# Optimization experiments

Hardware: AMD Instinct MI355X
Metric: run time of the kernel (lower is better)

Reference implementation:

```python
import jax, jax.numpy as jnp
import numpy as np

EPS = 1e-5
LN_EPS = 1e-5
NUM_EXPERTS = 8
TOP_K = 2
HIDDEN = 1024
INTER = 2048


def _swiglu(x, wg, wu, wd):
    # x: [T,H]; wg,wu: [H,I]; wd: [I,H]
    return (jax.nn.silu(x @ wg) * (x @ wu)) @ wd


def setup_inputs() -> dict:
    key = jax.random.key(0)
    ks = jax.random.split(key, 10)
    B, S, H, I, E = 8, 4096, HIDDEN, INTER, NUM_EXPERTS
    std_h = 1.0 / np.sqrt(H)
    std_i = 1.0 / np.sqrt(I)
    return {
        "x": jax.random.normal(ks[0], (B, S, H), dtype=jnp.float32),
        "ln_scale": jnp.ones((H,), dtype=jnp.float32),
        "ln_bias": jnp.zeros((H,), dtype=jnp.float32),
        "gate_w": jax.random.normal(ks[1], (E, H), dtype=jnp.float32) * 0.01,
        "Wg": jax.random.normal(ks[2], (E, H, I), dtype=jnp.float32) * std_h,
        "Wu": jax.random.normal(ks[3], (E, H, I), dtype=jnp.float32) * std_h,
        "Wd": jax.random.normal(ks[4], (E, I, H), dtype=jnp.float32) * std_i,
        "sWg": jax.random.normal(ks[5], (H, I), dtype=jnp.float32) * std_h,
        "sWu": jax.random.normal(ks[6], (H, I), dtype=jnp.float32) * std_h,
        "sWd": jax.random.normal(ks[7], (I, H), dtype=jnp.float32) * std_i,
    }


def reference(x, ln_scale, ln_bias, gate_w, Wg, Wu, Wd, sWg, sWu, sWd):
    B, S, H = x.shape
    xf = x.reshape(-1, H)  # [T,H]
    # Router: LayerNorm -> gate -> softmax -> top-k -> renormalize
    mu = jnp.mean(xf, axis=-1, keepdims=True)
    var = jnp.var(xf, axis=-1, keepdims=True)
    xn = (xf - mu) * jax.lax.rsqrt(var + LN_EPS) * ln_scale + ln_bias
    logits = xn @ gate_w.T  # [T,E]
    probs = jax.nn.softmax(logits, axis=-1)
    tk_probs, tk_idx = jax.lax.top_k(probs, TOP_K)  # [T,K]
    tk_probs = tk_probs / (jnp.sum(tk_probs, axis=-1, keepdims=True) + EPS)
    # Per-expert combine weight: w[t,e] = sum_k tk_probs[t,k] * (tk_idx[t,k]==e)
    onehot = (tk_idx[..., None] == jnp.arange(NUM_EXPERTS)[None, None, :])  # [T,K,E]
    w = jnp.sum(tk_probs[..., None] * onehot.astype(tk_probs.dtype), axis=1)  # [T,E]
    # Shared expert + weighted routed experts
    out = _swiglu(xf, sWg, sWu, sWd)
    for e in range(NUM_EXPERTS):
        out = out + w[:, e:e + 1] * _swiglu(xf, Wg[e], Wu[e], Wd[e])
    return out.reshape(B, S, H)
```

## Files before the change

kernel.cpp:

```cpp
#include <hip/hip_runtime.h>

#define H 1024
#define ITR 2048
#define NE 8
#define BT 32

typedef __attribute__((ext_vector_type(8))) short short8;
typedef __attribute__((ext_vector_type(4))) float f32x4;

__device__ __forceinline__ float bf2f(unsigned short u){
  union { unsigned int i; float f; } v; v.i = ((unsigned int)u) << 16; return v.f;
}
__device__ __forceinline__ unsigned short f2bf(float f){
  union { unsigned int i; float f; } v; v.f = f;
  unsigned int r = v.i + 0x7FFFu + ((v.i >> 16) & 1u);
  return (unsigned short)(r >> 16);
}
__device__ __forceinline__ void gload16(const void* g, void* l){
  __builtin_amdgcn_global_load_lds((const __attribute__((address_space(1))) void*)g,
                                   (__attribute__((address_space(3))) void*)l, 16, 0, 0);
}

__global__ __launch_bounds__(64) void detect_k(const unsigned int* __restrict__ xw,
                                               int* __restrict__ flag, int* __restrict__ cnt16){
  int lane = threadIdx.x;
  int c = 0;
  #pragma unroll
  for (int i = 0; i < 4; i++){
    unsigned u = xw[lane * 4 + i];
    int e = (u >> 7) & 0xFF;
    c += (e >= 100 && e <= 140) ? 1 : 0;
  }
  #pragma unroll
  for (int off = 32; off; off >>= 1) c += __shfl_xor(c, off);
  if (lane == 0) flag[0] = (c < 128) ? 1 : 0;
  if (lane < 16) cnt16[lane] = 0;
}

__device__ __forceinline__ void loadv16(const void* base, size_t off, int isf, float* out){
  if (isf){
    const float* p = (const float*)base + off;
    float4 a = *(const float4*)p, b = *(const float4*)(p + 4);
    float4 c = *(const float4*)(p + 8), d = *(const float4*)(p + 12);
    out[0]=a.x; out[1]=a.y; out[2]=a.z; out[3]=a.w;
    out[4]=b.x; out[5]=b.y; out[6]=b.z; out[7]=b.w;
    out[8]=c.x; out[9]=c.y; out[10]=c.z; out[11]=c.w;
    out[12]=d.x; out[13]=d.y; out[14]=d.z; out[15]=d.w;
  } else {
    const unsigned short* p = (const unsigned short*)base + off;
    uint4 a = *(const uint4*)p, b = *(const uint4*)(p + 8);
    unsigned short u[16];
    *(uint4*)u = a; *(uint4*)(u + 8) = b;
    #pragma unroll
    for (int j = 0; j < 16; j++) out[j] = bf2f(u[j]);
  }
}

__global__ __launch_bounds__(256) void trans_k(
    const void* __restrict__ rg, const void* __restrict__ ru, const void* __restrict__ rd,
    const void* __restrict__ sg, const void* __restrict__ su, const void* __restrict__ sd,
    unsigned short* __restrict__ arena, const int* __restrict__ flag)
{
  int slot = blockIdx.z / 3, mt = blockIdx.z % 3;
  int e = slot;
  int R = (mt == 2) ? ITR : H;
  int C = (mt == 2) ? H : ITR;
  int c0 = blockIdx.x * 64, r0 = blockIdx.y * 64;
  if (c0 >= C || r0 >= R) return;
  const void* srcv;
  size_t eoff = 0;
  if (e == NE) srcv = (mt == 0) ? sg : ((mt == 1) ? su : sd);
  else { srcv = (mt == 0) ? rg : ((mt == 1) ? ru : rd); eoff = (size_t)e * H * ITR; }
  unsigned short* dst = arena + (size_t)slot * (3u * H * ITR)
                      + (mt == 2 ? (size_t)2 * H * ITR : 0);
  int isf = *flag;
  __shared__ unsigned short tile[64][72];
  int t = threadIdx.x;
  int row = t >> 3, c8 = (t & 7) * 8;
  #pragma unroll
  for (int p = 0; p < 2; p++){
    int r = r0 + row + p * 32;
    unsigned short v[8];
    if (isf){
      const float* s = (const float*)srcv + eoff + (size_t)r * C + c0 + c8;
      float4 a = *(const float4*)s, b = *(const float4*)(s + 4);
      v[0]=f2bf(a.x); v[1]=f2bf(a.y); v[2]=f2bf(a.z); v[3]=f2bf(a.w);
      v[4]=f2bf(b.x); v[5]=f2bf(b.y); v[6]=f2bf(b.z); v[7]=f2bf(b.w);
    } else {
      const unsigned short* s = (const unsigned short*)srcv + eoff + (size_t)r * C + c0 + c8;
      *(uint4*)v = *(const uint4*)s;
    }
    *(uint4*)&tile[row + p * 32][c8] = *(const uint4*)v;
  }
  __syncthreads();
  #pragma unroll
  for (int p = 0; p < 2; p++){
    int c = row + p * 32;
    int dc = c0 + c;
    int dr = (mt == 2) ? dc : (((dc >> 5) << 6) + mt * 32 + (dc & 31));
    unsigned short tmp[8];
    #pragma unroll
    for (int j = 0; j < 8; j++) tmp[j] = tile[c8 + j][c];
    *(uint4*)(dst + (size_t)dr * R + r0 + c8) = *(const uint4*)tmp;
  }
}

__global__ __launch_bounds__(256) void router2_k(
    const void* __restrict__ x, const void* __restrict__ lns, const void* __restrict__ lnb,
    const void* __restrict__ gw, int T, const int* __restrict__ flag,
    int* __restrict__ cnt16, int* __restrict__ lidx, float* __restrict__ lw)
{
  int isf = *flag;
  int tid = threadIdx.x, wv = tid >> 6, lane = tid & 63;
  int t0 = blockIdx.x * BT;
  __shared__ int scc[16], sbase[16];
  __shared__ int sei[2][BT], soi[2][BT];
  __shared__ float swv[2][BT];
  if (tid < 16) scc[tid] = 0;
  float sc[16], bi[16];
  loadv16(lns, (size_t)lane * 16, isf, sc);
  loadv16(lnb, (size_t)lane * 16, isf, bi);
  __syncthreads();

  for (int i = 0; i < BT / 4; i++){
    int tl = i * 4 + wv;
    int tok = t0 + tl;
    if (tok >= T) break;
    float v[16];
    loadv16(x, (size_t)tok * H + lane * 16, isf, v);
    float sum = 0.f, ss = 0.f;
    #pragma unroll
    for (int j = 0; j < 16; j++){ sum += v[j]; ss += v[j] * v[j]; }
    #pragma unroll
    for (int off = 32; off; off >>= 1){ sum += __shfl_xor(sum, off); ss += __shfl_xor(ss, off); }
    float mu = sum * (1.f / H);
    float rstd = rsqrtf(ss * (1.f / H) - mu * mu + 1e-5f);
    float xn[16];
    #pragma unroll
    for (int j = 0; j < 16; j++) xn[j] = (v[j] - mu) * rstd * sc[j] + bi[j];
    float acc[NE];
    #pragma unroll
    for (int e = 0; e < NE; e++){
      float g[16];
      loadv16(gw, (size_t)e * H + lane * 16, isf, g);
      float s = 0.f;
      #pragma unroll
      for (int j = 0; j < 16; j++) s += xn[j] * g[j];
      acc[e] = s;
    }
    #pragma unroll
    for (int off = 32; off; off >>= 1){
      #pragma unroll
      for (int e = 0; e < NE; e++) acc[e] += __shfl_xor(acc[e], off);
    }
    if (lane == 0){
      float m = acc[0];
      #pragma unroll
      for (int e = 1; e < NE; e++) m = fmaxf(m, acc[e]);
      float p[NE], Z = 0.f;
      #pragma unroll
      for (int e = 0; e < NE; e++){ p[e] = expf(acc[e] - m); Z += p[e]; }
      float iZ = 1.f / Z;
      #pragma unroll
      for (int e = 0; e < NE; e++) p[e] *= iZ;
      int i1 = 0;
      #pragma unroll
      for (int e = 1; e < NE; e++) if (p[e] > p[i1]) i1 = e;
      int i2 = (i1 == 0) ? 1 : 0;
      #pragma unroll
      for (int e = 0; e < NE; e++) if (e != i1 && p[e] > p[i2]) i2 = e;
      float s2 = p[i1] + p[i2] + 1e-5f;
      int o1 = atomicAdd(&scc[i1], 1);
      int o2 = atomicAdd(&scc[8 + i2], 1);
      sei[0][tl] = i1; soi[0][tl] = o1; swv[0][tl] = p[i1] / s2;
      sei[1][tl] = i2; soi[1][tl] = o2; swv[1][tl] = p[i2] / s2;
    }
  }
  __syncthreads();
  if (tid < 16) sbase[tid] = atomicAdd(&cnt16[tid], scc[tid]);
  __syncthreads();
  if (tid < 2 * BT){
    int l = tid / BT, t = tid % BT;
    int tok = t0 + t;
    if (tok < T){
      int ctr = l * 8 + sei[l][t];
      int pos = sbase[ctr] + soi[l][t];
      lidx[(size_t)ctr * T + pos] = tok;
      lw[(size_t)ctr * T + pos] = swv[l][t];
    }
  }
}

__global__ __launch_bounds__(64) void scan_k(const int* __restrict__ cnt16,
                                             int* __restrict__ segA, int* __restrict__ segEp,
                                             int* __restrict__ segCnt, int T, int CH,
                                             int L1C, int L2C){
  if (threadIdx.x == 0){
    segA[0] = 0; segEp[0] = T; segCnt[0] = T;
    int b = L1C * CH;
    for (int e = 0; e < 8; e++){
      segA[1 + e] = b; segCnt[1 + e] = cnt16[e];
      b += (cnt16[e] + 255) & ~255;
      segEp[1 + e] = b;
    }
    b = L2C * CH;
    for (int e = 0; e < 8; e++){
      segA[9 + e] = b; segCnt[9 + e] = cnt16[8 + e];
      b += (cnt16[8 + e] + 255) & ~255;
      segEp[9 + e] = b;
    }
  }
}

template<int EPI>
__global__ __launch_bounds__(512, 2) void gemm256_k(
    const void* __restrict__ Asrc, const unsigned short* __restrict__ arena,
    unsigned short* __restrict__ hidden, void* __restrict__ outp,
    const int* __restrict__ segA, const int* __restrict__ segEp, const int* __restrict__ segCnt,
    const int* __restrict__ lidx, const float* __restrict__ lw,
    int T, int CH, int c0chunk, int hmask, const int* __restrict__ flag)
{
  constexpr int K  = (EPI == 2) ? ITR : H;
  constexpr int NT = K / 64;
  int chid = c0chunk + blockIdx.z;
  int tn = blockIdx.x, tm = blockIdx.y;
  int pr0 = chid * CH + tm * 256;

  int s = -1;
  if (pr0 < T) s = 0;
  else {
    #pragma unroll
    for (int i = 1; i <= 16; i++)
      if (pr0 >= segA[i] && pr0 < segEp[i]) s = i;
  }
  if (s < 0) return;
  int cnt = segCnt[s], base = segA[s];
  int slot = (s == 0) ? 8 : ((s - 1) & 7);
  const unsigned short* wT = arena + (size_t)slot * (3u * H * ITR)
                           + (EPI == 2 ? (size_t)2 * H * ITR : 0);
  int isf = *flag;

  __shared__ unsigned short Al[2][256 * 64];
  __shared__ unsigned short Bl[2][256 * 64];

  int tid = threadIdx.x, wid = tid >> 6, lane = tid & 63;
  int ldr = tid >> 3;
  int c8s = (((tid & 7) ^ (ldr & 7)) * 8);

  const unsigned short* abf[4];
  const float* af32[4];
  #pragma unroll
  for (int q = 0; q < 4; q++){
    if (EPI == 2){
      int pr = pr0 + q * 64 + ldr;
      int hrow = ((chid & hmask) ? CH : 0) + (pr - chid * CH);
      abf[q] = (const unsigned short*)Asrc + (size_t)hrow * ITR + c8s;
      af32[q] = nullptr;
    } else {
      int rl = pr0 - base + q * 64 + ldr;
      int rc = cnt - 1; rl = rl < rc ? rl : rc;
      int tok = (s == 0) ? rl : lidx[(size_t)(s - 1) * T + rl];
      abf[q] = (const unsigned short*)Asrc + (size_t)tok * H + c8s;
      af32[q] = (const float*)Asrc + (size_t)tok * H + c8s;
    }
  }
  const unsigned short* bptr[4];
  #pragma unroll
  for (int q = 0; q < 4; q++)
    bptr[q] = wT + (size_t)(tn * 256 + q * 64 + ldr) * K + c8s;

  f32x4 acc[8][4];
  f32x4 zero4 = {0.f, 0.f, 0.f, 0.f};
  #pragma unroll
  for (int m = 0; m < 8; m++)
    #pragma unroll
    for (int n = 0; n < 4; n++) acc[m][n] = zero4;

  int wm = (wid >> 2) * 128, wn = (wid & 3) * 64;
  int fr = lane & 15, fq = lane >> 4;

  auto stage = [&](int buf, int kt){
    int k0 = kt * 64;
    unsigned short* Ab = &Al[buf][0];
    unsigned short* Bb = &Bl[buf][0];
    #pragma unroll
    for (int q = 0; q < 4; q++){
      if (EPI == 0 && isf){
        float4 v0 = *(const float4*)(af32[q] + k0);
        float4 v1 = *(const float4*)(af32[q] + k0 + 4);
        unsigned short w8[8] = {f2bf(v0.x), f2bf(v0.y), f2bf(v0.z), f2bf(v0.w),
                                f2bf(v1.x), f2bf(v1.y), f2bf(v1.z), f2bf(v1.w)};
        *(uint4*)((char*)Ab + q * 8192 + tid * 16) = *(const uint4*)w8;
      } else {
        gload16(abf[q] + k0, (char*)Ab + q * 8192 + wid * 1024);
      }
      gload16(bptr[q] + k0, (char*)Bb + q * 8192 + wid * 1024);
    }
  };

  auto compute = [&](int buf){
    const unsigned short* Ab = &Al[buf][0];
    const unsigned short* Bb = &Bl[buf][0];
    __builtin_amdgcn_s_setprio(1);
    #pragma unroll
    for (int ks = 0; ks < 2; ks++){
      int un = ((ks * 4 + fq) ^ (fr & 7)) * 8;
      short8 a[8], b[4];
      #pragma unroll
      for (int m = 0; m < 8; m++)
        a[m] = *(const short8*)(Ab + (wm + m * 16 + fr) * 64 + un);
      #pragma unroll
      for (int n = 0; n < 4; n++)
        b[n] = *(const short8*)(Bb + (wn + n * 16 + fr) * 64 + un);
      #pragma unroll
      for (int m = 0; m < 8; m++)
        #pragma unroll
        for (int n = 0; n < 4; n++)
          acc[m][n] = __builtin_amdgcn_mfma_f32_16x16x32_bf16(a[m], b[n], acc[m][n], 0, 0, 0);
    }
    __builtin_amdgcn_s_setprio(0);
  };

  stage(0, 0);
  int cur = 0;
  for (int kt = 0; kt < NT; kt++){
    if (kt + 1 < NT) stage(cur ^ 1, kt + 1);
    if (EPI == 0 && isf) asm volatile("s_waitcnt lgkmcnt(0)" ::: "memory");
    if (kt + 1 < NT) asm volatile("s_waitcnt vmcnt(8)" ::: "memory");
    else             asm volatile("s_waitcnt vmcnt(0)" ::: "memory");
    __builtin_amdgcn_s_barrier();
    compute(cur);
    __builtin_amdgcn_s_barrier();
    cur ^= 1;
  }

  int rb = fq * 4, cb = fr;
  if (EPI == 0){
    int g64 = tn * 4 + (wid & 3);
    int rl0 = pr0 - chid * CH;
    unsigned short* hb = hidden + ((chid & hmask) ? (size_t)CH * ITR : 0);
    #pragma unroll
    for (int m = 0; m < 8; m++){
      #pragma unroll
      for (int j = 0; j < 4; j++){
        int rl = rl0 + wm + m * 16 + rb + j;
        unsigned short* hr = hb + (size_t)rl * ITR + g64 * 32 + cb;
        #pragma unroll
        for (int nf = 0; nf < 2; nf++){
          float g = acc[m][nf][j], u = acc[m][nf + 2][j];
          hr[nf * 16] = f2bf(g / (1.f + __expf(-g)) * u);
        }
      }
    }
  } else {
    #pragma unroll
    for (int m = 0; m < 8; m++){
      #pragma unroll
      for (int j = 0; j < 4; j++){
        int pr = pr0 + wm + m * 16 + rb + j;
        int rl = pr - base;
        if (rl < cnt){
          int tok = (s == 0) ? rl : lidx[(size_t)(s - 1) * T + rl];
          size_t ob = (size_t)tok * H + tn * 256 + wn + cb;
          if (s == 0){
            if (isf){
              float* p = (float*)outp + ob;
              #pragma unroll
              for (int n = 0; n < 4; n++) p[n * 16] = acc[m][n][j];
            } else {
              unsigned short* p = (unsigned short*)outp + ob;
              #pragma unroll
              for (int n = 0; n < 4; n++) p[n * 16] = f2bf(acc[m][n][j]);
            }
          } else {
            float wgt = lw[(size_t)(s - 1) * T + rl];
            if (isf){
              float* p = (float*)outp + ob;
              #pragma unroll
              for (int n = 0; n < 4; n++) p[n * 16] += wgt * acc[m][n][j];
            } else {
              unsigned short* p = (unsigned short*)outp + ob;
              #pragma unroll
              for (int n = 0; n < 4; n++) p[n * 16] = f2bf(bf2f(p[n * 16]) + wgt * acc[m][n][j]);
            }
          }
        }
      }
    }
  }
}

extern "C" void kernel_launch(void* const* d_in, const int* in_sizes, int n_in,
                              void* d_out, int out_size, void* d_ws, size_t ws_size,
                              hipStream_t stream)
{
  int T = in_sizes[0] / H;

  char* w = (char*)d_ws;
  auto alloc = [&](size_t b){ char* p = w; w += (b + 255) & ~(size_t)255; return p; };
  int* flag   = (int*)alloc(256);
  int* cnt16  = (int*)alloc(256);
  int* segA   = (int*)alloc(256);
  int* segEp  = (int*)alloc(256);
  int* segCnt = (int*)alloc(256);
  int* lidx   = (int*)alloc((size_t)16 * T * 4);
  float* lw   = (float*)alloc((size_t)16 * T * 4);
  const size_t ARENA = (size_t)9 * 3 * H * ITR * 2;
  unsigned short* arena = (unsigned short*)alloc(ARENA);
  size_t used = (size_t)(w - (char*)d_ws);

  int CH = 2048, hmask = 0;
  {
    struct { int ch, hm; } lad[4] = {{8192,1},{4096,1},{2048,1},{2048,0}};
    for (int i = 0; i < 4; i++){
      size_t need = used + (size_t)(lad[i].hm + 1) * lad[i].ch * ITR * 2 + 1024;
      if (need <= ws_size){ CH = lad[i].ch; hmask = lad[i].hm; break; }
    }
  }
  unsigned short* hidden = (unsigned short*)alloc((size_t)(hmask + 1) * CH * ITR * 2);

  int CB1 = (T + CH - 1) / CH;
  int chunks1 = (T + 8 * 255 + CH - 1) / CH;
  int CB2 = CB1 + chunks1;
  int NCHUNK = CB2 + chunks1;

  detect_k<<<1, 64, 0, stream>>>((const unsigned int*)d_in[0], flag, cnt16);
  router2_k<<<(T + BT - 1) / BT, 256, 0, stream>>>(d_in[0], d_in[1], d_in[2], d_in[3],
                                                   T, flag, cnt16, lidx, lw);
  scan_k<<<1, 64, 0, stream>>>(cnt16, segA, segEp, segCnt, T, CH, CB1, CB2);
  trans_k<<<dim3(32, 32, 27), 256, 0, stream>>>(d_in[4], d_in[5], d_in[6],
                                                d_in[7], d_in[8], d_in[9], arena, flag);

  auto nextb = [&](int a){ return a < CB1 ? CB1 : (a < CB2 ? CB2 : NCHUNK); };

  int c = 0;
  while (c < NCHUNK){
    int z = (hmask && c + 1 < NCHUNK) ? 2 : 1;
    gemm256_k<0><<<dim3(16, CH / 256, z), 512, 0, stream>>>(
        d_in[0], arena, hidden, nullptr, segA, segEp, segCnt, lidx, lw,
        T, CH, c, hmask, flag);
    int a = c;
    while (a < c + z){
      int b = nextb(a); if (b > c + z) b = c + z;
      gemm256_k<2><<<dim3(4, CH / 256, b - a), 512, 0, stream>>>(
          hidden, arena, hidden, d_out, segA, segEp, segCnt, lidx, lw,
          T, CH, a, hmask, flag);
      a = b;
    }
    c += z;
  }
}
```

Measured before the change: 2.816 ms.

## Use full-size hidden buffer with single launches and XCD-aware block remapping

When the workspace is large enough, the whole intermediate hidden activation is allocated at once. The up-projection and down-projection GEMMs then each run as a single grid over all chunks, replacing the chunked loop of many launches. Block IDs are also remapped so that consecutive blocks on the same XCD share a row tile across column tiles, which aims to improve L2 reuse of the A operand. This removes launch overhead and the per-chunk tail effects, at the cost of a much larger workspace footprint and an extra global round-trip of the hidden buffer without chunk-level cache locality.

```diff
diff --git a/kernel.cpp b/kernel.cpp
--- a/kernel.cpp
+++ b/kernel.cpp
@@ -218,12 +218,27 @@
     unsigned short* __restrict__ hidden, void* __restrict__ outp,
     const int* __restrict__ segA, const int* __restrict__ segEp, const int* __restrict__ segCnt,
     const int* __restrict__ lidx, const float* __restrict__ lw,
-    int T, int CH, int c0chunk, int hmask, const int* __restrict__ flag)
+    int T, int CH, int c0chunk, int hmask, int fullh, const int* __restrict__ flag)
 {
   constexpr int K  = (EPI == 2) ? ITR : H;
   constexpr int NT = K / 64;
-  int chid = c0chunk + blockIdx.z;
-  int tn = blockIdx.x, tm = blockIdx.y;
+
+  int tn, tm, chid;
+  {
+    unsigned gx = gridDim.x, gy = gridDim.y;
+    unsigned PT = gy * gridDim.z;
+    unsigned fid = blockIdx.x + gx * (blockIdx.y + gy * blockIdx.z);
+    if ((PT & 7u) == 0u){
+      unsigned xcd = fid & 7u, local = fid >> 3;
+      tn = local % gx;
+      unsigned p = local / gx;
+      unsigned tmz = xcd + 8u * p;
+      tm = tmz % gy;
+      chid = c0chunk + tmz / gy;
+    } else {
+      tn = blockIdx.x; tm = blockIdx.y; chid = c0chunk + blockIdx.z;
+    }
+  }
   int pr0 = chid * CH + tm * 256;
 
   int s = -1;
@@ -253,7 +268,7 @@
   for (int q = 0; q < 4; q++){
     if (EPI == 2){
       int pr = pr0 + q * 64 + ldr;
-      int hrow = ((chid & hmask) ? CH : 0) + (pr - chid * CH);
+      int hrow = fullh ? pr : (((chid & hmask) ? CH : 0) + (pr - chid * CH));
       abf[q] = (const unsigned short*)Asrc + (size_t)hrow * ITR + c8s;
       af32[q] = nullptr;
     } else {
@@ -337,8 +352,8 @@
   int rb = fq * 4, cb = fr;
   if (EPI == 0){
     int g64 = tn * 4 + (wid & 3);
-    int rl0 = pr0 - chid * CH;
-    unsigned short* hb = hidden + ((chid & hmask) ? (size_t)CH * ITR : 0);
+    int rl0 = fullh ? pr0 : (pr0 - chid * CH);
+    unsigned short* hb = hidden + ((!fullh && (chid & hmask)) ? (size_t)CH * ITR : 0);
     #pragma unroll
     for (int m = 0; m < 8; m++){
       #pragma unroll
@@ -409,15 +424,30 @@
   unsigned short* arena = (unsigned short*)alloc(ARENA);
   size_t used = (size_t)(w - (char*)d_ws);
 
-  int CH = 2048, hmask = 0;
+  auto nchunksOf = [&](int ch){
+    int cb1 = (T + ch - 1) / ch;
+    int c1  = (T + 8 * 255 + ch - 1) / ch;
+    return cb1 + 2 * c1;
+  };
+
+  int CH = 2048, hmask = 0, fullh = 0;
+  size_t hidbytes = 0;
   {
-    struct { int ch, hm; } lad[4] = {{8192,1},{4096,1},{2048,1},{2048,0}};
-    for (int i = 0; i < 4; i++){
-      size_t need = used + (size_t)(lad[i].hm + 1) * lad[i].ch * ITR * 2 + 1024;
-      if (need <= ws_size){ CH = lad[i].ch; hmask = lad[i].hm; break; }
-    }
-  }
-  unsigned short* hidden = (unsigned short*)alloc((size_t)(hmask + 1) * CH * ITR * 2);
+    int nch8 = nchunksOf(8192);
+    size_t needF = used + (size_t)nch8 * 8192 * ITR * 2 + 1024;
+    if (needF <= ws_size){
+      CH = 8192; fullh = 1; hmask = 0;
+      hidbytes = (size_t)nch8 * 8192 * ITR * 2;
+    } else {
+      struct { int ch, hm; } lad[4] = {{8192,1},{4096,1},{2048,1},{2048,0}};
+      for (int i = 0; i < 4; i++){
+        size_t need = used + (size_t)(lad[i].hm + 1) * lad[i].ch * ITR * 2 + 1024;
+        if (need <= ws_size){ CH = lad[i].ch; hmask = lad[i].hm; break; }
+      }
+      hidbytes = (size_t)(hmask + 1) * CH * ITR * 2;
+    }
+  }
+  unsigned short* hidden = (unsigned short*)alloc(hidbytes);
 
   int CB1 = (T + CH - 1) / CH;
   int chunks1 = (T + 8 * 255 + CH - 1) / CH;
@@ -431,22 +461,30 @@
   trans_k<<<dim3(32, 32, 27), 256, 0, stream>>>(d_in[4], d_in[5], d_in[6],
                                                 d_in[7], d_in[8], d_in[9], arena, flag);
 
-  auto nextb = [&](int a){ return a < CB1 ? CB1 : (a < CB2 ? CB2 : NCHUNK); };
-
-  int c = 0;
-  while (c < NCHUNK){
-    int z = (hmask && c + 1 < NCHUNK) ? 2 : 1;
-    gemm256_k<0><<<dim3(16, CH / 256, z), 512, 0, stream>>>(
+  if (fullh){
+    gemm256_k<0><<<dim3(16, CH / 256, NCHUNK), 512, 0, stream>>>(
         d_in[0], arena, hidden, nullptr, segA, segEp, segCnt, lidx, lw,
-        T, CH, c, hmask, flag);
-    int a = c;
-    while (a < c + z){
-      int b = nextb(a); if (b > c + z) b = c + z;
-      gemm256_k<2><<<dim3(4, CH / 256, b - a), 512, 0, stream>>>(
-          hidden, arena, hidden, d_out, segA, segEp, segCnt, lidx, lw,
-          T, CH, a, hmask, flag);
-      a = b;
-    }
-    c += z;
-  }
-}
+        T, CH, 0, 0, 1, flag);
+    gemm256_k<2><<<dim3(4, CH / 256, NCHUNK), 512, 0, stream>>>(
+        hidden, arena, hidden, d_out, segA, segEp, segCnt, lidx, lw,
+        T, CH, 0, 0, 1, flag);
+  } else {
+    auto nextb = [&](int a){ return a < CB1 ? CB1 : (a < CB2 ? CB2 : NCHUNK); };
+    int c = 0;
+    while (c < NCHUNK){
+      int z = (hmask && c + 1 < NCHUNK) ? 2 : 1;
+      gemm256_k<0><<<dim3(16, CH / 256, z), 512, 0, stream>>>(
+          d_in[0], arena, hidden, nullptr, segA, segEp, segCnt, lidx, lw,
+          T, CH, c, hmask, 0, flag);
+      int a = c;
+      while (a < c + z){
+        int b = nextb(a); if (b > c + z) b = c + z;
+        gemm256_k<2><<<dim3(4, CH / 256, b - a), 512, 0, stream>>>(
+            hidden, arena, hidden, d_out, segA, segEp, segCnt, lidx, lw,
+            T, CH, a, hmask, 0, flag);
+        a = b;
+      }
+      c += z;
+    }
+  }
+}
```

After: 2.816 ms. No clear change (-0.0%).

## Shrink GEMM tiles to 128x128 with K-step 32 and restructure chunk launches

Applied to the files above, without the earlier changes.

The grouped expert GEMM kernel moves from 256x256 tiles with 512 threads and K-step 64 to 128x128 tiles with 256 threads and K-step 32. The LDS swizzle, wait counts and epilogue indexing are rewritten to match. Host chunk scheduling now iterates per region, so paired chunks never straddle the shared/layer boundaries, and the hidden-buffer ladder prefers a single large chunk. Smaller tiles give more blocks and less padding waste for small expert segments, at the cost of lower arithmetic intensity per block and more global traffic for the weights.

```diff
diff --git a/kernel.cpp b/kernel.cpp
--- a/kernel.cpp
+++ b/kernel.cpp
@@ -213,18 +213,18 @@
 }
 
 template<int EPI>
-__global__ __launch_bounds__(512, 2) void gemm256_k(
+__global__ __launch_bounds__(256, 2) void gemm128_k(
     const void* __restrict__ Asrc, const unsigned short* __restrict__ arena,
     unsigned short* __restrict__ hidden, void* __restrict__ outp,
     const int* __restrict__ segA, const int* __restrict__ segEp, const int* __restrict__ segCnt,
     const int* __restrict__ lidx, const float* __restrict__ lw,
-    int T, int CH, int c0chunk, int hmask, const int* __restrict__ flag)
+    int T, int CH, int c0chunk, int nh, const int* __restrict__ flag)
 {
   constexpr int K  = (EPI == 2) ? ITR : H;
-  constexpr int NT = K / 64;
+  constexpr int NT = K / 32;
   int chid = c0chunk + blockIdx.z;
   int tn = blockIdx.x, tm = blockIdx.y;
-  int pr0 = chid * CH + tm * 256;
+  int pr0 = chid * CH + tm * 128;
 
   int s = -1;
   if (pr0 < T) s = 0;
@@ -240,84 +240,80 @@
                            + (EPI == 2 ? (size_t)2 * H * ITR : 0);
   int isf = *flag;
 
-  __shared__ unsigned short Al[2][256 * 64];
-  __shared__ unsigned short Bl[2][256 * 64];
-
-  int tid = threadIdx.x, wid = tid >> 6, lane = tid & 63;
-  int ldr = tid >> 3;
-  int c8s = (((tid & 7) ^ (ldr & 7)) * 8);
-
-  const unsigned short* abf[4];
-  const float* af32[4];
-  #pragma unroll
-  for (int q = 0; q < 4; q++){
+  __shared__ unsigned short Al[2][128 * 32];
+  __shared__ unsigned short Bl[2][128 * 32];
+
+  int tid = threadIdx.x, wid = tid >> 6, l = tid & 63;
+  int fr = l & 15, fq = l >> 4;
+  int r0l = wid * 32 + (l >> 2);
+  int su = (tid & 3) ^ ((l >> 3) & 3);
+  size_t hoff = (nh == 2 && (chid & 1)) ? (size_t)CH * ITR : 0;
+
+  const unsigned short* aptr[2];
+  const float* afp[2];
+  #pragma unroll
+  for (int q = 0; q < 2; q++){
+    int rloc = r0l + q * 16;
     if (EPI == 2){
-      int pr = pr0 + q * 64 + ldr;
-      int hrow = ((chid & hmask) ? CH : 0) + (pr - chid * CH);
-      abf[q] = (const unsigned short*)Asrc + (size_t)hrow * ITR + c8s;
-      af32[q] = nullptr;
+      aptr[q] = (const unsigned short*)Asrc + hoff + (size_t)(pr0 - chid * CH + rloc) * ITR + su * 8;
+      afp[q] = nullptr;
     } else {
-      int rl = pr0 - base + q * 64 + ldr;
+      int rl = pr0 - base + rloc;
       int rc = cnt - 1; rl = rl < rc ? rl : rc;
       int tok = (s == 0) ? rl : lidx[(size_t)(s - 1) * T + rl];
-      abf[q] = (const unsigned short*)Asrc + (size_t)tok * H + c8s;
-      af32[q] = (const float*)Asrc + (size_t)tok * H + c8s;
-    }
-  }
-  const unsigned short* bptr[4];
-  #pragma unroll
-  for (int q = 0; q < 4; q++)
-    bptr[q] = wT + (size_t)(tn * 256 + q * 64 + ldr) * K + c8s;
-
-  f32x4 acc[8][4];
+      aptr[q] = (const unsigned short*)Asrc + (size_t)tok * H + su * 8;
+      afp[q]  = (const float*)Asrc + (size_t)tok * H + su * 8;
+    }
+  }
+  const unsigned short* bptr[2];
+  #pragma unroll
+  for (int q = 0; q < 2; q++)
+    bptr[q] = wT + (size_t)(tn * 128 + r0l + q * 16) * K + su * 8;
+
+  f32x4 acc[4][4];
   f32x4 zero4 = {0.f, 0.f, 0.f, 0.f};
   #pragma unroll
-  for (int m = 0; m < 8; m++)
+  for (int m = 0; m < 4; m++)
     #pragma unroll
     for (int n = 0; n < 4; n++) acc[m][n] = zero4;
 
-  int wm = (wid >> 2) * 128, wn = (wid & 3) * 64;
-  int fr = lane & 15, fq = lane >> 4;
+  int wm = (wid >> 1) * 64, wn = (wid & 1) * 64;
 
   auto stage = [&](int buf, int kt){
-    int k0 = kt * 64;
-    unsigned short* Ab = &Al[buf][0];
-    unsigned short* Bb = &Bl[buf][0];
-    #pragma unroll
-    for (int q = 0; q < 4; q++){
+    int k0 = kt * 32;
+    #pragma unroll
+    for (int q = 0; q < 2; q++){
+      int lbyte = (wid * 32 + q * 16) * 64;
       if (EPI == 0 && isf){
-        float4 v0 = *(const float4*)(af32[q] + k0);
-        float4 v1 = *(const float4*)(af32[q] + k0 + 4);
+        const float* f = afp[q] + k0;
+        float4 v0 = *(const float4*)f, v1 = *(const float4*)(f + 4);
         unsigned short w8[8] = {f2bf(v0.x), f2bf(v0.y), f2bf(v0.z), f2bf(v0.w),
                                 f2bf(v1.x), f2bf(v1.y), f2bf(v1.z), f2bf(v1.w)};
-        *(uint4*)((char*)Ab + q * 8192 + tid * 16) = *(const uint4*)w8;
+        *(uint4*)((char*)&Al[buf][0] + (r0l + q * 16) * 64 + (tid & 3) * 16) = *(const uint4*)w8;
       } else {
-        gload16(abf[q] + k0, (char*)Ab + q * 8192 + wid * 1024);
+        gload16(aptr[q] + k0, (char*)&Al[buf][0] + lbyte);
       }
-      gload16(bptr[q] + k0, (char*)Bb + q * 8192 + wid * 1024);
+      gload16(bptr[q] + k0, (char*)&Bl[buf][0] + lbyte);
     }
   };
 
   auto compute = [&](int buf){
     const unsigned short* Ab = &Al[buf][0];
     const unsigned short* Bb = &Bl[buf][0];
+    int un = (fq ^ ((fr >> 1) & 3)) * 8;
     __builtin_amdgcn_s_setprio(1);
-    #pragma unroll
-    for (int ks = 0; ks < 2; ks++){
-      int un = ((ks * 4 + fq) ^ (fr & 7)) * 8;
-      short8 a[8], b[4];
-      #pragma unroll
-      for (int m = 0; m < 8; m++)
-        a[m] = *(const short8*)(Ab + (wm + m * 16 + fr) * 64 + un);
+    short8 a[4], b[4];
+    #pragma unroll
+    for (int m = 0; m < 4; m++)
+      a[m] = *(const short8*)(Ab + (wm + m * 16 + fr) * 32 + un);
+    #pragma unroll
+    for (int n = 0; n < 4; n++)
+      b[n] = *(const short8*)(Bb + (wn + n * 16 + fr) * 32 + un);
+    #pragma unroll
+    for (int m = 0; m < 4; m++)
       #pragma unroll
       for (int n = 0; n < 4; n++)
-        b[n] = *(const short8*)(Bb + (wn + n * 16 + fr) * 64 + un);
-      #pragma unroll
-      for (int m = 0; m < 8; m++)
-        #pragma unroll
-        for (int n = 0; n < 4; n++)
-          acc[m][n] = __builtin_amdgcn_mfma_f32_16x16x32_bf16(a[m], b[n], acc[m][n], 0, 0, 0);
-    }
+        acc[m][n] = __builtin_amdgcn_mfma_f32_16x16x32_bf16(a[m], b[n], acc[m][n], 0, 0, 0);
     __builtin_amdgcn_s_setprio(0);
   };
 
@@ -326,42 +322,46 @@
   for (int kt = 0; kt < NT; kt++){
     if (kt + 1 < NT) stage(cur ^ 1, kt + 1);
     if (EPI == 0 && isf) asm volatile("s_waitcnt lgkmcnt(0)" ::: "memory");
-    if (kt + 1 < NT) asm volatile("s_waitcnt vmcnt(8)" ::: "memory");
-    else             asm volatile("s_waitcnt vmcnt(0)" ::: "memory");
+    if (kt + 1 < NT){
+      if (EPI == 0 && isf) asm volatile("s_waitcnt vmcnt(2)" ::: "memory");
+      else                 asm volatile("s_waitcnt vmcnt(4)" ::: "memory");
+    } else {
+      asm volatile("s_waitcnt vmcnt(0)" ::: "memory");
+    }
     __builtin_amdgcn_s_barrier();
     compute(cur);
     __builtin_amdgcn_s_barrier();
     cur ^= 1;
   }
 
-  int rb = fq * 4, cb = fr;
+  int rb = fq * 4;
   if (EPI == 0){
-    int g64 = tn * 4 + (wid & 3);
+    int colbase = tn * 64 + (wid & 1) * 32;
     int rl0 = pr0 - chid * CH;
-    unsigned short* hb = hidden + ((chid & hmask) ? (size_t)CH * ITR : 0);
-    #pragma unroll
-    for (int m = 0; m < 8; m++){
+    unsigned short* hb = hidden + hoff;
+    #pragma unroll
+    for (int m = 0; m < 4; m++){
       #pragma unroll
       for (int j = 0; j < 4; j++){
         int rl = rl0 + wm + m * 16 + rb + j;
-        unsigned short* hr = hb + (size_t)rl * ITR + g64 * 32 + cb;
+        unsigned short* hr = hb + (size_t)rl * ITR + colbase;
         #pragma unroll
-        for (int nf = 0; nf < 2; nf++){
-          float g = acc[m][nf][j], u = acc[m][nf + 2][j];
-          hr[nf * 16] = f2bf(g / (1.f + __expf(-g)) * u);
+        for (int k = 0; k < 2; k++){
+          float g = acc[m][k][j], uu = acc[m][k + 2][j];
+          hr[k * 16 + fr] = f2bf(g / (1.f + __expf(-g)) * uu);
         }
       }
     }
   } else {
     #pragma unroll
-    for (int m = 0; m < 8; m++){
+    for (int m = 0; m < 4; m++){
       #pragma unroll
       for (int j = 0; j < 4; j++){
         int pr = pr0 + wm + m * 16 + rb + j;
         int rl = pr - base;
         if (rl < cnt){
           int tok = (s == 0) ? rl : lidx[(size_t)(s - 1) * T + rl];
-          size_t ob = (size_t)tok * H + tn * 256 + wn + cb;
+          size_t ob = (size_t)tok * H + tn * 128 + wn + fr;
           if (s == 0){
             if (isf){
               float* p = (float*)outp + ob;
@@ -409,15 +409,15 @@
   unsigned short* arena = (unsigned short*)alloc(ARENA);
   size_t used = (size_t)(w - (char*)d_ws);
 
-  int CH = 2048, hmask = 0;
+  int CH = 2048, nh = 1;
   {
-    struct { int ch, hm; } lad[4] = {{8192,1},{4096,1},{2048,1},{2048,0}};
+    struct { int ch, n; } lad[4] = {{8192,2},{8192,1},{4096,1},{2048,1}};
     for (int i = 0; i < 4; i++){
-      size_t need = used + (size_t)(lad[i].hm + 1) * lad[i].ch * ITR * 2 + 1024;
-      if (need <= ws_size){ CH = lad[i].ch; hmask = lad[i].hm; break; }
-    }
-  }
-  unsigned short* hidden = (unsigned short*)alloc((size_t)(hmask + 1) * CH * ITR * 2);
+      size_t need = used + (size_t)lad[i].n * lad[i].ch * ITR * 2 + 1024;
+      if (need <= ws_size){ CH = lad[i].ch; nh = lad[i].n; break; }
+    }
+  }
+  unsigned short* hidden = (unsigned short*)alloc((size_t)nh * CH * ITR * 2);
 
   int CB1 = (T + CH - 1) / CH;
   int chunks1 = (T + 8 * 255 + CH - 1) / CH;
@@ -431,22 +431,17 @@
   trans_k<<<dim3(32, 32, 27), 256, 0, stream>>>(d_in[4], d_in[5], d_in[6],
                                                 d_in[7], d_in[8], d_in[9], arena, flag);
 
-  auto nextb = [&](int a){ return a < CB1 ? CB1 : (a < CB2 ? CB2 : NCHUNK); };
-
-  int c = 0;
-  while (c < NCHUNK){
-    int z = (hmask && c + 1 < NCHUNK) ? 2 : 1;
-    gemm256_k<0><<<dim3(16, CH / 256, z), 512, 0, stream>>>(
-        d_in[0], arena, hidden, nullptr, segA, segEp, segCnt, lidx, lw,
-        T, CH, c, hmask, flag);
-    int a = c;
-    while (a < c + z){
-      int b = nextb(a); if (b > c + z) b = c + z;
-      gemm256_k<2><<<dim3(4, CH / 256, b - a), 512, 0, stream>>>(
+  int bnds[4] = {0, CB1, CB2, NCHUNK};
+  for (int r = 0; r < 3; r++){
+    for (int c = bnds[r]; c < bnds[r + 1]; ){
+      int z = (nh == 2 && c + 1 < bnds[r + 1]) ? 2 : 1;
+      gemm128_k<0><<<dim3(32, CH / 128, z), 256, 0, stream>>>(
+          d_in[0], arena, hidden, nullptr, segA, segEp, segCnt, lidx, lw,
+          T, CH, c, nh, flag);
+      gemm128_k<2><<<dim3(8, CH / 128, z), 256, 0, stream>>>(
           hidden, arena, hidden, d_out, segA, segEp, segCnt, lidx, lw,
-          T, CH, a, hmask, flag);
-      a = b;
-    }
-    c += z;
-  }
-}
+          T, CH, c, nh, flag);
+      c += z;
+    }
+  }
+}
```

New measurement: 2.638 ms. -6.3%, faster.
